# Performance work log

Measured on AMD Instinct MI355X. Metric: run time of the kernel, lower is better.

Reference implementation:

```python
import jax, jax.numpy as jnp
import numpy as np

N_NODES = 50000
N_EDGES = 800000
D_FEAT = 64
D_HID = 64
N_CLASSES = 16


def gcn_conv(x, row, col, ew, W, b, n_nodes):
    """PyG GCNConv (normalize=True, add_self_loops=True) with edge weights.
    out[c] = sum_{(r,c) in E+selfloops} d^-1/2[r] * w * d^-1/2[c] * (x @ W)[r] + b
    """
    h = x @ W  # [N, out]
    loop = jnp.arange(n_nodes)
    row = jnp.concatenate([row, loop])
    col = jnp.concatenate([col, loop])
    w = jnp.concatenate([ew, jnp.ones((n_nodes,), dtype=ew.dtype)])
    deg = jax.ops.segment_sum(w, col, num_segments=n_nodes)  # in-degree (weighted)
    dinv = jnp.where(deg > 0, jax.lax.rsqrt(deg), 0.0)
    norm = dinv[row] * w * dinv[col]  # [E+N]
    msgs = norm[:, None] * h[row]  # [E+N, out]
    out = jax.ops.segment_sum(msgs, col, num_segments=n_nodes)
    return out + b


def setup_inputs() -> dict:
    key = jax.random.key(0)
    ks = jax.random.split(key, 12)
    x = jax.random.normal(ks[0], (N_NODES, D_FEAT), dtype=jnp.float32)
    edge_index = jax.random.randint(ks[1], (2, N_EDGES), 0, N_NODES, dtype=jnp.int64)
    edge_attr = jax.random.uniform(ks[2], (N_EDGES,), dtype=jnp.float32)
    s1 = 1.0 / np.sqrt(D_FEAT)
    s2 = 1.0 / np.sqrt(D_HID)
    W1 = jax.random.uniform(ks[3], (D_FEAT, D_HID), minval=-s1, maxval=s1, dtype=jnp.float32)
    b1 = jnp.zeros((D_HID,), dtype=jnp.float32)
    W2 = jax.random.uniform(ks[4], (D_HID, D_HID), minval=-s2, maxval=s2, dtype=jnp.float32)
    b2 = jnp.zeros((D_HID,), dtype=jnp.float32)
    Wm1 = jax.random.uniform(ks[5], (D_HID, D_HID), minval=-s2, maxval=s2, dtype=jnp.float32)
    bm1 = jax.random.uniform(ks[6], (D_HID,), minval=-s2, maxval=s2, dtype=jnp.float32)
    Wm2 = jax.random.uniform(ks[7], (D_HID, N_CLASSES), minval=-s2, maxval=s2, dtype=jnp.float32)
    bm2 = jax.random.uniform(ks[8], (N_CLASSES,), minval=-s2, maxval=s2, dtype=jnp.float32)
    return {"x": x, "edge_index": edge_index, "edge_attr": edge_attr,
            "W1": W1, "b1": b1, "W2": W2, "b2": b2,
            "Wm1": Wm1, "bm1": bm1, "Wm2": Wm2, "bm2": bm2}


def reference(x, edge_index, edge_attr, W1, b1, W2, b2, Wm1, bm1, Wm2, bm2):
    # eval-mode forward: dropout is identity
    n = x.shape[0]
    row, col = edge_index[0], edge_index[1]
    h = jax.nn.relu(gcn_conv(x, row, col, edge_attr, W1, b1, n))
    h = jax.nn.relu(gcn_conv(h, row, col, edge_attr, W2, b2, n))
    h = jax.nn.relu(h @ Wm1 + bm1)
    logits = h @ Wm2 + bm2
    return jax.nn.sigmoid(logits)
```

## Files before the change

kernel.cpp:

```cpp
#include <hip/hip_runtime.h>
#include <hip/hip_fp16.h>
#include <math.h>

#define D 64
#define CAP 48
#define PSZ 256
#define NBIN 196
#define BCAP 4864
#define TSTRIDE 16
#define FILLB 1024
#define MMBLK 2048
#define ITMAX 4
#define EWINV (1.0f / 65535.0f)
#define GNODES 16
#define ROWU4 (CAP / 4)
#define STU4  (GNODES * ROWU4)

typedef unsigned long long u64;
typedef unsigned uint4v __attribute__((ext_vector_type(4)));


__global__ void __launch_bounds__(256, 2) k_mm1_fill(
        const float* __restrict__ X, const float* __restrict__ W1,
        __half* __restrict__ Y, int n, int mmBlocks,
        const int* __restrict__ row, const int* __restrict__ col,
        const float* __restrict__ ew, int* __restrict__ tails,
        u64* __restrict__ binsG, int E) {
    __shared__ int hist[NBIN], startS[NBIN], curS[NBIN], baseS[NBIN];
    __shared__ int gsum[16];

    if (blockIdx.x < FILLB) {
        int fb  = blockIdx.x;
        int tid = threadIdx.x;
        int chunk = (E + FILLB - 1) / FILLB;
        int e0 = fb * chunk;
        int e1 = min(e0 + chunk, E);

        for (int i = tid; i < NBIN; i += 256) hist[i] = 0;
        __syncthreads();

        unsigned lov[ITMAX], ewv[ITMAX];
        unsigned char binv[ITMAX];
#pragma unroll
        for (int it = 0; it < ITMAX; ++it) {
            int e = e0 + it * 256 + tid;
            if (e < e1) {
                int c = col[e];
                int bn = c >> 8;
                binv[it] = (unsigned char)bn;
                lov[it]  = ((unsigned)row[e] << 8) | (unsigned)(c & (PSZ - 1));
                ewv[it]  = __float_as_uint(ew[e]);
                atomicAdd(&hist[bn], 1);
            }
        }
        __syncthreads();
        if (tid < 13) {
            int s = 0, hi = min(tid * 16 + 16, NBIN);
            for (int i = tid * 16; i < hi; ++i) s += hist[i];
            gsum[tid] = s;
        }
        __syncthreads();
        if (tid < NBIN) {
            int s = 0, g = tid >> 4;
            for (int i = 0; i < g; ++i) s += gsum[i];
            for (int i = g << 4; i < tid; ++i) s += hist[i];
            startS[tid] = s;
            curS[tid]   = s;
            baseS[tid]  = atomicAdd(&tails[tid * TSTRIDE], hist[tid]);
        }
        __syncthreads();
#pragma unroll
        for (int it = 0; it < ITMAX; ++it) {
            int e = e0 + it * 256 + tid;
            if (e < e1) {
                int bn = binv[it];
                int p  = atomicAdd(&curS[bn], 1);
                int dst = baseS[bn] + (p - startS[bn]);
                if (dst < BCAP)
                    binsG[(size_t)bn * BCAP + dst] = ((u64)ewv[it] << 32) | lov[it];
            }
        }
    } else {
        int lane = threadIdx.x & 63;
        float wreg[64];
#pragma unroll
        for (int k = 0; k < 64; ++k) wreg[k] = W1[k * 64 + lane];
        int wv  = (blockIdx.x - FILLB) * 4 + (threadIdx.x >> 6);
        int nwv = mmBlocks * 4;
        const float4* x4 = (const float4*)X;
        for (int r = wv; r < n; r += nwv) {
            float acc0 = 0.f, acc1 = 0.f;
#pragma unroll
            for (int j = 0; j < 8; ++j) {
                float4 v = x4[r * 16 + j];
                acc0 += v.x * wreg[4 * j + 0] + v.y * wreg[4 * j + 1]
                      + v.z * wreg[4 * j + 2] + v.w * wreg[4 * j + 3];
            }
#pragma unroll
            for (int j = 8; j < 16; ++j) {
                float4 v = x4[r * 16 + j];
                acc1 += v.x * wreg[4 * j + 0] + v.y * wreg[4 * j + 1]
                      + v.z * wreg[4 * j + 2] + v.w * wreg[4 * j + 3];
            }
            Y[r * 64 + lane] = __float2half(acc0 + acc1);
        }
    }
}


__global__ void k_binscatter(const u64* __restrict__ binsG,
                             const int* __restrict__ tails,
                             int* __restrict__ cnt, float* __restrict__ dinv,
                             unsigned* __restrict__ bucket, __half* __restrict__ xw1, int n) {
    __shared__ int   lc[PSZ];
    __shared__ float lsum[PSZ];
    int bin = blockIdx.x, tid = threadIdx.x;
    for (int i = tid; i < PSZ; i += blockDim.x) { lc[i] = 0; lsum[i] = 0.f; }
    __syncthreads();
    int m = tails[bin * TSTRIDE];
    if (m > BCAP) m = BCAP;
    const u64* src = binsG + (size_t)bin * BCAP;
    int base = bin * PSZ;
    for (int i = tid; i < m; i += blockDim.x) {
        u64 v = __builtin_nontemporal_load(&src[i]);
        unsigned lo = (unsigned)v;
        int cOff = lo & (PSZ - 1);
        unsigned r = (lo >> 8) & 0xFFFF;
        float wv = __uint_as_float((unsigned)(v >> 32));
        float qf = rintf(wv * 65535.0f);
        int p = atomicAdd(&lc[cOff], 1);
        atomicAdd(&lsum[cOff], qf);
        if (p < CAP)
            bucket[(size_t)(base + cOff) * CAP + p] = ((unsigned)qf << 16) | r;
    }
    __syncthreads();
    for (int i = tid; i < PSZ; i += blockDim.x) {
        int node = base + i;
        if (node < n) {
            int c = lc[i];
            cnt[node] = c;
            float dv = rsqrtf(1.0f + lsum[i] * EWINV);
            dinv[node] = dv;
            lsum[i] = dv;
            int cA = min(c, CAP);
            int cB = min(lc[i ^ 1], CAP);
            int cm8 = (max(cA, cB) + 7) & ~7;
            unsigned* brow = bucket + (size_t)node * CAP;
            for (int j = cA; j < cm8; ++j) brow[j] = 0u;
        }
    }
    __syncthreads();
    int lim = min(PSZ, n - base);
    float4* x4 = (float4*)(xw1 + (size_t)base * 64);
    for (int idx = tid; idx < lim * 8; idx += blockDim.x) {
        float dv = lsum[idx >> 3];
        float4 raw = x4[idx];
        __half2* h = (__half2*)&raw;
#pragma unroll
        for (int j = 0; j < 4; ++j) {
            float lo = __half2float(__low2half(h[j]))  * dv;
            float hi = __half2float(__high2half(h[j])) * dv;
            h[j] = __halves2half2(__float2half(lo), __float2half(hi));
        }
        x4[idx] = raw;
    }
}


__device__ __forceinline__ void gather_pair(const __half* __restrict__ xw,
                                            const unsigned* ep, int cm8, int li,
                                            float dd, float bbx, float bby,
                                            int myNode, float& r0, float& r1) {
    const unsigned* xwu = (const unsigned*)xw;
    unsigned su = xwu[(size_t)myNode * 32 + li];
    __half2 sh = *(__half2*)&su;
    float s0 = __half2float(__low2half(sh));
    float s1 = __half2float(__high2half(sh));
    float a0 = 0.f, a1 = 0.f, b0 = 0.f, b1 = 0.f;
    for (int j = 0; j < cm8; j += 8) {
        unsigned q0 = ep[j + 0], q1 = ep[j + 1], q2 = ep[j + 2], q3 = ep[j + 3];
        unsigned q4 = ep[j + 4], q5 = ep[j + 5], q6 = ep[j + 6], q7 = ep[j + 7];
        unsigned u0 = xwu[(size_t)(q0 & 0xFFFFu) * 32 + li];
        unsigned u1 = xwu[(size_t)(q1 & 0xFFFFu) * 32 + li];
        unsigned u2 = xwu[(size_t)(q2 & 0xFFFFu) * 32 + li];
        unsigned u3 = xwu[(size_t)(q3 & 0xFFFFu) * 32 + li];
        unsigned u4 = xwu[(size_t)(q4 & 0xFFFFu) * 32 + li];
        unsigned u5 = xwu[(size_t)(q5 & 0xFFFFu) * 32 + li];
        unsigned u6 = xwu[(size_t)(q6 & 0xFFFFu) * 32 + li];
        unsigned u7 = xwu[(size_t)(q7 & 0xFFFFu) * 32 + li];
        __half2 h0 = *(__half2*)&u0, h1 = *(__half2*)&u1, h2 = *(__half2*)&u2, h3 = *(__half2*)&u3;
        __half2 h4 = *(__half2*)&u4, h5 = *(__half2*)&u5, h6 = *(__half2*)&u6, h7 = *(__half2*)&u7;
        float w0 = (float)(q0 >> 16), w1 = (float)(q1 >> 16);
        float w2 = (float)(q2 >> 16), w3 = (float)(q3 >> 16);
        float w4 = (float)(q4 >> 16), w5 = (float)(q5 >> 16);
        float w6 = (float)(q6 >> 16), w7 = (float)(q7 >> 16);
        a0 += w0 * __half2float(__low2half(h0));  a1 += w0 * __half2float(__high2half(h0));
        b0 += w1 * __half2float(__low2half(h1));  b1 += w1 * __half2float(__high2half(h1));
        a0 += w2 * __half2float(__low2half(h2));  a1 += w2 * __half2float(__high2half(h2));
        b0 += w3 * __half2float(__low2half(h3));  b1 += w3 * __half2float(__high2half(h3));
        a0 += w4 * __half2float(__low2half(h4));  a1 += w4 * __half2float(__high2half(h4));
        b0 += w5 * __half2float(__low2half(h5));  b1 += w5 * __half2float(__high2half(h5));
        a0 += w6 * __half2float(__low2half(h6));  a1 += w6 * __half2float(__high2half(h6));
        b0 += w7 * __half2float(__low2half(h7));  b1 += w7 * __half2float(__high2half(h7));
    }
    r0 = dd * (s0 + EWINV * (a0 + b0)) + bbx;
    r1 = dd * (s1 + EWINV * (a1 + b1)) + bby;
}


__global__ void __launch_bounds__(256) k_gather_mm(
        const __half* __restrict__ xw, const float* __restrict__ dinv,
        const float* __restrict__ b, const int* __restrict__ cnt,
        const unsigned* __restrict__ bucket, const float* __restrict__ W,
        __half* __restrict__ out, int n) {
    __shared__ float ws[64][64];
    __shared__ float hs[4][2][64];
    __shared__ unsigned ebuf[2][GNODES][CAP];
    __shared__ int   cbuf[2][GNODES];
    __shared__ float dbuf[2][GNODES];
    int tid = threadIdx.x, lane = tid & 63, w = tid >> 6;
    int hi = lane >> 5, li = lane & 31;
    for (int i = tid; i < 4096; i += 256) ws[i >> 6][i & 63] = W[i];
    float2 bbv = ((const float2*)b)[li];

    int ngg = (n + GNODES - 1) / GNODES;
    int gg = blockIdx.x;
    if (gg < ngg) {
        int base = gg * GNODES;
        int lim = min(GNODES, n - base);
        if (tid < lim * ROWU4)
            ((uint4v*)&ebuf[0][0][0])[tid] =
                __builtin_nontemporal_load((const uint4v*)(bucket + (size_t)base * CAP) + tid);
        if (tid >= STU4 && tid - STU4 < lim)        cbuf[0][tid - STU4] = cnt[base + tid - STU4];
        if (tid >= STU4 + 16 && tid - STU4 - 16 < lim) dbuf[0][tid - STU4 - 16] = dinv[base + tid - STU4 - 16];
    }
    __syncthreads();
    int cur = 0;
    while (gg < ngg) {
        int ggN = gg + gridDim.x;
        bool haveN = (ggN < ngg);
        uint4v nE = (uint4v)(0u); int nC = 0; float nD = 0.f; int limN = 0;
        if (haveN) {
            int baseN = ggN * GNODES;
            limN = min(GNODES, n - baseN);
            if (tid < limN * ROWU4)
                nE = __builtin_nontemporal_load((const uint4v*)(bucket + (size_t)baseN * CAP) + tid);
            if (tid >= STU4 && tid - STU4 < limN)        nC = cnt[baseN + tid - STU4];
            if (tid >= STU4 + 16 && tid - STU4 - 16 < limN) nD = dinv[baseN + tid - STU4 - 16];
        }
        int base = gg * GNODES;
#pragma unroll
        for (int p = 0; p < 2; ++p) {
            int ln0 = w * 4 + p * 2;
            int myLn = ln0 + hi;
            int myNode = base + myLn;
            if (myNode < n) {
                int cA = cbuf[cur][ln0];     if (cA > CAP) cA = CAP;
                int cB = cbuf[cur][ln0 + 1]; if (cB > CAP) cB = CAP;
                int cm8 = (max(cA, cB) + 7) & ~7;
                float dd = dbuf[cur][myLn];
                float r0, r1;
                gather_pair(xw, &ebuf[cur][myLn][0], cm8, li, dd, bbv.x, bbv.y, myNode, r0, r1);
                *(float2*)&hs[w][hi][2 * li] = make_float2(fmaxf(r0, 0.f), fmaxf(r1, 0.f));
                __builtin_amdgcn_wave_barrier();
                float s0 = 0.f, s1 = 0.f;
#pragma unroll
                for (int k = 0; k < 64; ++k) {
                    float hk = hs[w][hi][k];
                    float2 wk = *(const float2*)&ws[k][2 * li];
                    s0 += hk * wk.x;  s1 += hk * wk.y;
                }
                __builtin_amdgcn_wave_barrier();
                __half2 oh = __halves2half2(__float2half(dd * s0), __float2half(dd * s1));
                ((unsigned*)out)[(size_t)myNode * 32 + li] = *(unsigned*)&oh;
            }
        }
        if (!haveN) break;
        __syncthreads();
        if (tid < limN * ROWU4) ((uint4v*)&ebuf[cur ^ 1][0][0])[tid] = nE;
        if (tid >= STU4 && tid - STU4 < limN)        cbuf[cur ^ 1][tid - STU4] = nC;
        if (tid >= STU4 + 16 && tid - STU4 - 16 < limN) dbuf[cur ^ 1][tid - STU4 - 16] = nD;
        __syncthreads();
        gg = ggN; cur ^= 1;
    }
}


__global__ void __launch_bounds__(256) k_gather_head(
        const __half* __restrict__ xw, const float* __restrict__ dinv,
        const float* __restrict__ b, const int* __restrict__ cnt,
        const unsigned* __restrict__ bucket,
        const float* __restrict__ Wm1, const float* __restrict__ bm1,
        const float* __restrict__ Wm2, const float* __restrict__ bm2,
        float* __restrict__ out, int n) {
    __shared__ __half w1h[64][64];
    __shared__ float w2[64][16];
    __shared__ float sb2[16];
    __shared__ float h2s[4][2][64];
    __shared__ float h3s[4][2][64];
    __shared__ unsigned ebuf[2][GNODES][CAP];
    __shared__ int   cbuf[2][GNODES];
    __shared__ float dbuf[2][GNODES];
    int tid = threadIdx.x, lane = tid & 63, w = tid >> 6;
    int hi = lane >> 5, li = lane & 31;
    for (int i = tid; i < 4096; i += 256) w1h[i >> 6][i & 63] = __float2half(Wm1[i]);
    for (int i = tid; i < 1024; i += 256) w2[i >> 4][i & 15] = Wm2[i];
    if (tid < 16) sb2[tid] = bm2[tid];
    float2 bbv  = ((const float2*)b)[li];
    float2 bb1v = ((const float2*)bm1)[li];

    int ngg = (n + GNODES - 1) / GNODES;
    int gg = blockIdx.x;
    if (gg < ngg) {
        int base = gg * GNODES;
        int lim = min(GNODES, n - base);
        if (tid < lim * ROWU4)
            ((uint4v*)&ebuf[0][0][0])[tid] =
                __builtin_nontemporal_load((const uint4v*)(bucket + (size_t)base * CAP) + tid);
        if (tid >= STU4 && tid - STU4 < lim)        cbuf[0][tid - STU4] = cnt[base + tid - STU4];
        if (tid >= STU4 + 16 && tid - STU4 - 16 < lim) dbuf[0][tid - STU4 - 16] = dinv[base + tid - STU4 - 16];
    }
    __syncthreads();
    int cur = 0;
    while (gg < ngg) {
        int ggN = gg + gridDim.x;
        bool haveN = (ggN < ngg);
        uint4v nE = (uint4v)(0u); int nC = 0; float nD = 0.f; int limN = 0;
        if (haveN) {
            int baseN = ggN * GNODES;
            limN = min(GNODES, n - baseN);
            if (tid < limN * ROWU4)
                nE = __builtin_nontemporal_load((const uint4v*)(bucket + (size_t)baseN * CAP) + tid);
            if (tid >= STU4 && tid - STU4 < limN)        nC = cnt[baseN + tid - STU4];
            if (tid >= STU4 + 16 && tid - STU4 - 16 < limN) nD = dinv[baseN + tid - STU4 - 16];
        }
        int base = gg * GNODES;
#pragma unroll
        for (int p = 0; p < 2; ++p) {
            int ln0 = w * 4 + p * 2;
            int myLn = ln0 + hi;
            int myNode = base + myLn;
            if (myNode < n) {
                int cA = cbuf[cur][ln0];     if (cA > CAP) cA = CAP;
                int cB = cbuf[cur][ln0 + 1]; if (cB > CAP) cB = CAP;
                int cm8 = (max(cA, cB) + 7) & ~7;
                float dd = dbuf[cur][myLn];
                float r0, r1;
                gather_pair(xw, &ebuf[cur][myLn][0], cm8, li, dd, bbv.x, bbv.y, myNode, r0, r1);
                *(float2*)&h2s[w][hi][2 * li] = make_float2(fmaxf(r0, 0.f), fmaxf(r1, 0.f));
                __builtin_amdgcn_wave_barrier();
                float s0 = bb1v.x, s1 = bb1v.y;
#pragma unroll
                for (int k = 0; k < 64; ++k) {
                    float hk = h2s[w][hi][k];
                    unsigned wu = *(const unsigned*)&w1h[k][2 * li];
                    __half2 wh = *(__half2*)&wu;
                    s0 += hk * __half2float(__low2half(wh));
                    s1 += hk * __half2float(__high2half(wh));
                }
                *(float2*)&h3s[w][hi][2 * li] = make_float2(fmaxf(s0, 0.f), fmaxf(s1, 0.f));
                __builtin_amdgcn_wave_barrier();
                if (li < 16) {
                    float s2 = sb2[li];
#pragma unroll
                    for (int k = 0; k < 64; ++k) s2 += h3s[w][hi][k] * w2[k][li];
                    out[(size_t)myNode * 16 + li] = 1.0f / (1.0f + expf(-s2));
                }
                __builtin_amdgcn_wave_barrier();
            }
        }
        if (!haveN) break;
        __syncthreads();
        if (tid < limN * ROWU4) ((uint4v*)&ebuf[cur ^ 1][0][0])[tid] = nE;
        if (tid >= STU4 && tid - STU4 < limN)        cbuf[cur ^ 1][tid - STU4] = nC;
        if (tid >= STU4 + 16 && tid - STU4 - 16 < limN) dbuf[cur ^ 1][tid - STU4 - 16] = nD;
        __syncthreads();
        gg = ggN; cur ^= 1;
    }
}


extern "C" void kernel_launch(void* const* d_in, const int* in_sizes, int n_in,
                              void* d_out, int out_size, void* d_ws, size_t ws_size,
                              hipStream_t stream) {
    const float* x   = (const float*)d_in[0];
    const int*   ei  = (const int*)d_in[1];
    const float* ew  = (const float*)d_in[2];
    const float* W1  = (const float*)d_in[3];
    const float* b1  = (const float*)d_in[4];
    const float* W2  = (const float*)d_in[5];
    const float* b2  = (const float*)d_in[6];
    const float* Wm1 = (const float*)d_in[7];
    const float* bm1 = (const float*)d_in[8];
    const float* Wm2 = (const float*)d_in[9];
    const float* bm2 = (const float*)d_in[10];

    int n = in_sizes[0] / D;
    int E = in_sizes[1] / 2;
    const int* row = ei;
    const int* col = ei + E;

    char* wsb = (char*)d_ws;
    unsigned* bucket = (unsigned*)wsb;
    __half* xw1    = (__half*)(bucket + (size_t)n * CAP);
    u64*    binsG  = (u64*)(xw1 + (size_t)n * D);
    __half* xw2    = (__half*)binsG;
    int*    cnt    = (int*)(binsG + (size_t)NBIN * BCAP);
    float*  dinv   = (float*)(cnt + n);
    int*    tails  = (int*)(dinv + n);
    float*  outp   = (float*)d_out;

    (void)hipMemsetAsync(tails, 0, (size_t)NBIN * TSTRIDE * sizeof(int), stream);
    k_mm1_fill<<<FILLB + MMBLK, 256, 0, stream>>>(x, W1, xw1, n, MMBLK,
                                                  row, col, ew, tails, binsG, E);
    k_binscatter<<<NBIN, 512, 0, stream>>>(binsG, tails, cnt, dinv, bucket, xw1, n);
    k_gather_mm<<<1536, 256, 0, stream>>>(xw1, dinv, b1, cnt, bucket, W2, xw2, n);
    k_gather_head<<<1536, 256, 0, stream>>>(xw2, dinv, b2, cnt, bucket,
                                            Wm1, bm1, Wm2, bm2, outp, n);
}
```

Baseline: 227.2 us.

## Stage edge binning in shared memory and write bins with coalesced per-bin copies

```diff
diff --git a/kernel.cpp b/kernel.cpp
--- a/kernel.cpp
+++ b/kernel.cpp
@@ -8,9 +8,8 @@
 #define NBIN 196
 #define BCAP 4864
 #define TSTRIDE 16
-#define FILLB 1024
-#define MMBLK 2048
-#define ITMAX 4
+#define FILLB 128
+#define CHUNKMAX 6272
 #define EWINV (1.0f / 65535.0f)
 #define GNODES 16
 #define ROWU4 (CAP / 4)
@@ -26,8 +25,9 @@
         const int* __restrict__ row, const int* __restrict__ col,
         const float* __restrict__ ew, int* __restrict__ tails,
         u64* __restrict__ binsG, int E) {
+    __shared__ u64 buf[CHUNKMAX];
     __shared__ int hist[NBIN], startS[NBIN], curS[NBIN], baseS[NBIN];
-    __shared__ int gsum[16];
+    __shared__ int gsum[13];
 
     if (blockIdx.x < FILLB) {
         int fb  = blockIdx.x;
@@ -38,21 +38,8 @@
 
         for (int i = tid; i < NBIN; i += 256) hist[i] = 0;
         __syncthreads();
-
-        unsigned lov[ITMAX], ewv[ITMAX];
-        unsigned char binv[ITMAX];
-#pragma unroll
-        for (int it = 0; it < ITMAX; ++it) {
-            int e = e0 + it * 256 + tid;
-            if (e < e1) {
-                int c = col[e];
-                int bn = c >> 8;
-                binv[it] = (unsigned char)bn;
-                lov[it]  = ((unsigned)row[e] << 8) | (unsigned)(c & (PSZ - 1));
-                ewv[it]  = __float_as_uint(ew[e]);
-                atomicAdd(&hist[bn], 1);
-            }
-        }
+        for (int e = e0 + tid; e < e1; e += 256)
+            atomicAdd(&hist[col[e] >> 8], 1);
         __syncthreads();
         if (tid < 13) {
             int s = 0, hi = min(tid * 16 + 16, NBIN);
@@ -69,15 +56,23 @@
             baseS[tid]  = atomicAdd(&tails[tid * TSTRIDE], hist[tid]);
         }
         __syncthreads();
-#pragma unroll
-        for (int it = 0; it < ITMAX; ++it) {
-            int e = e0 + it * 256 + tid;
-            if (e < e1) {
-                int bn = binv[it];
-                int p  = atomicAdd(&curS[bn], 1);
-                int dst = baseS[bn] + (p - startS[bn]);
-                if (dst < BCAP)
-                    binsG[(size_t)bn * BCAP + dst] = ((u64)ewv[it] << 32) | lov[it];
+        for (int e = e0 + tid; e < e1; e += 256) {
+            int c = col[e];
+            int b = c >> 8;
+            int p = atomicAdd(&curS[b], 1);
+            buf[p] = ((u64)__float_as_uint(ew[e]) << 32)
+                   | ((unsigned)row[e] << 8) | (unsigned)(c & (PSZ - 1));
+        }
+        __syncthreads();
+        int wv = tid >> 6, lane = tid & 63;
+        for (int b = wv; b < NBIN; b += 4) {
+            int cb   = hist[b];
+            int src0 = startS[b];
+            int dst0 = baseS[b];
+            u64* dstp = binsG + (size_t)b * BCAP;
+            for (int j = lane; j < cb; j += 64) {
+                int dst = dst0 + j;
+                if (dst < BCAP) dstp[dst] = buf[src0 + j];
             }
         }
     } else {
@@ -410,10 +405,12 @@
     int*    tails  = (int*)(dinv + n);
     float*  outp   = (float*)d_out;
 
+    int mmBlocks = 1024;
+
     (void)hipMemsetAsync(tails, 0, (size_t)NBIN * TSTRIDE * sizeof(int), stream);
-    k_mm1_fill<<<FILLB + MMBLK, 256, 0, stream>>>(x, W1, xw1, n, MMBLK,
-                                                  row, col, ew, tails, binsG, E);
-    k_binscatter<<<NBIN, 512, 0, stream>>>(binsG, tails, cnt, dinv, bucket, xw1, n);
+    k_mm1_fill<<<FILLB + mmBlocks, 256, 0, stream>>>(x, W1, xw1, n, mmBlocks,
+                                                     row, col, ew, tails, binsG, E);
+    k_binscatter<<<NBIN, 1024, 0, stream>>>(binsG, tails, cnt, dinv, bucket, xw1, n);
     k_gather_mm<<<1536, 256, 0, stream>>>(xw1, dinv, b1, cnt, bucket, W2, xw2, n);
     k_gather_head<<<1536, 256, 0, stream>>>(xw2, dinv, b2, cnt, bucket,
                                             Wm1, bm1, Wm2, bm2, outp, n);
```

After: 203.5 us. 10.4% less time.
